# Optimization experiments

Hardware: AMD Instinct MI355X
Metric: run time of the kernel (lower is better)

## Reference

```python
import jax, jax.numpy as jnp
import numpy as np

FEATURE_W = 1.0
TRIPLET_W = 1.0
SOFT_W = 1.0
MARGIN = 0.2
TEMP = 1.0
COMMIT_W = 0.1
DISTORT_W = 0.1
STRIDE = 320

B, T, D, K = 8, 1500, 512, 4096


def setup_inputs() -> dict:
    key = jax.random.key(0)
    k1, k2, k3, k4, k5 = jax.random.split(key, 5)
    return {
        "student_features": jax.random.normal(k1, (B, T, D), dtype=jnp.float32),
        "teacher_features": jax.random.normal(k2, (B, T, D), dtype=jnp.float32),
        "teacher_codes": jax.random.randint(k3, (B, T), 0, K),
        "codebook": jax.random.normal(k4, (K, D), dtype=jnp.float32),
        "lengths": jax.random.randint(k5, (B,), 0, T * STRIDE),
    }


def _sq_dists(flat, codebook):
    x2 = jnp.sum(flat * flat, axis=-1, keepdims=True)          # (N,1)
    c2 = jnp.sum(codebook * codebook, axis=-1)[None, :]        # (1,K)
    xc = jnp.einsum("nd,kd->nk", flat, codebook)               # (N,K)
    return jnp.maximum(x2 + c2 - 2.0 * xc, 0.0)


def reference(student_features, teacher_features, teacher_codes, codebook, lengths):
    b, t, d = student_features.shape
    # valid-frame mask from sample lengths
    valid = jnp.minimum(lengths // STRIDE, t)                  # (B,)
    mask = (jnp.arange(t)[None, :] < valid[:, None]).astype(student_features.dtype)  # (B,T)
    msum = jnp.sum(mask)

    # feature loss: masked mean of per-token MSE
    diff = student_features - teacher_features
    feature_loss = jnp.sum(jnp.mean(diff * diff, axis=-1) * mask) / msum

    # triplet loss
    pos_dist = jnp.sqrt(jnp.sum(diff * diff, axis=-1))
    neg_teacher = jnp.roll(teacher_features, shift=1, axis=0)
    nd = student_features - neg_teacher
    neg_dist = jnp.sqrt(jnp.sum(nd * nd, axis=-1))
    triplet = jax.nn.relu(pos_dist - neg_dist + MARGIN)
    triplet_loss = jnp.sum(triplet * mask) / msum

    # soft token (KL distillation over codebook logits)
    s_flat = student_features.reshape(-1, d)                   # (B*T, D)
    t_flat = teacher_features.reshape(-1, d)
    s_logits = -_sq_dists(s_flat, codebook) / TEMP             # (B*T, K)
    t_logits = -_sq_dists(t_flat, codebook) / TEMP
    s_logp = jax.nn.log_softmax(s_logits, axis=-1)
    t_logp = jax.nn.log_softmax(t_logits, axis=-1)
    t_prob = jax.lax.stop_gradient(jnp.exp(t_logp))
    t_logp = jax.lax.stop_gradient(t_logp)
    kl_per_token = jnp.sum(t_prob * (t_logp - s_logp), axis=-1)  # (B*T,)
    flat_mask = mask.reshape(-1)
    soft_loss = jnp.sum(kl_per_token * flat_mask) / msum

    # VQ commitment / distortion (nearest-code quantization)
    codes = jnp.argmax(s_logits, axis=-1)                       # argmin dist == argmax logits
    quantized = codebook[codes].reshape(b, t, d)
    cdiff = student_features - jax.lax.stop_gradient(quantized)
    commitment_loss = jnp.mean(cdiff * cdiff)
    ddiff = jax.lax.stop_gradient(student_features) - quantized
    distortion_loss = jnp.mean(ddiff * ddiff)

    total = (FEATURE_W * feature_loss + TRIPLET_W * triplet_loss
             + SOFT_W * soft_loss + COMMIT_W * commitment_loss
             + DISTORT_W * distortion_loss)
    return total
```

## Files before the change

### kernel.cpp

```cpp
#include <hip/hip_runtime.h>

typedef unsigned short u16;
typedef unsigned int   u32;
typedef float  f32x16 __attribute__((ext_vector_type(16)));
typedef __bf16 bf16x8 __attribute__((ext_vector_type(8)));

#define B_N   8
#define T_N   1500
#define D_N   512
#define K_N   4096
#define NTOK  12000
#define STRD  320

#define X2S_OFF     0u
#define C2_OFF      49152u
#define FEATP_OFF   65536u
#define TRIPP_OFF   67584u
#define SOFTP2_OFF  69632u
#define COMMP2_OFF  70656u
#define STATEP_OFF  71680u
#define SBF_OFF     557056u
#define TBF_OFF     (557056u + 12288000u)
#define CBBF_OFF    (557056u + 24576000u)


__device__ __forceinline__ u16 f2bf(float x){
  u32 u = __float_as_uint(x);
  u32 r = (u + 0x7fffu + ((u >> 16) & 1u)) >> 16;
  return (u16)r;
}

__device__ __forceinline__ void gl_lds16(const void* g, void* l){
  __builtin_amdgcn_global_load_lds(
      (__attribute__((address_space(1))) void*)(g),
      (__attribute__((address_space(3))) void*)(l),
      16, 0, 0);
}

__device__ __forceinline__ void merge_state(float& m, float& Z, float om, float oZ){
  float nm = fmaxf(m, om);
  Z = Z*__expf(m - nm) + oZ*__expf(om - nm);
  m = nm;
}
__device__ __forceinline__ void merge_stateT(float& m, float& Z, float& A,
                                             float om, float oZ, float oA){
  float nm = fmaxf(m, om);
  float e0 = __expf(m - nm), e1 = __expf(om - nm);
  Z = Z*e0 + oZ*e1; A = A*e0 + oA*e1; m = nm;
}

__global__ __launch_bounds__(256) void prep_feat_kernel(
    const float* __restrict__ s, const float* __restrict__ t,
    const int* __restrict__ lengths,
    u16* __restrict__ sbf, u16* __restrict__ tbf,
    float* __restrict__ x2s, float* __restrict__ featP, float* __restrict__ tripP)
{
  const int tid = threadIdx.x;
  const int w = tid >> 6, lane = tid & 63;
  const int kh = lane >> 5, sp = lane & 31;
  const int tt = blockIdx.x;
  const int n = tt*32 + sp;
  const int b = n / T_N, tok = n - b*T_N;
  const int nr = ((b+7)&7)*T_N + tok;
  const float* srow = s + (size_t)n  * D_N;
  const float* trow = t + (size_t)n  * D_N;
  const float* rrow = t + (size_t)nr * D_N;

  float x2 = 0.f, sd2 = 0.f, nd2 = 0.f;
#pragma unroll
  for (int j = 0; j < 8; ++j){
    const int ks = w*8 + j;
    const int k0 = ks*16 + kh*8;
    float4 s0 = *(const float4*)(srow + k0), s1 = *(const float4*)(srow + k0 + 4);
    float4 t0 = *(const float4*)(trow + k0), t1 = *(const float4*)(trow + k0 + 4);
    float4 r0 = *(const float4*)(rrow + k0), r1 = *(const float4*)(rrow + k0 + 4);
    float sv[8] = {s0.x,s0.y,s0.z,s0.w,s1.x,s1.y,s1.z,s1.w};
    float tv[8] = {t0.x,t0.y,t0.z,t0.w,t1.x,t1.y,t1.z,t1.w};
    float rv[8] = {r0.x,r0.y,r0.z,r0.w,r1.x,r1.y,r1.z,r1.w};
    u16 sb[8], tb[8];
#pragma unroll
    for (int i = 0; i < 8; ++i){
      float d = sv[i] - tv[i]; sd2 += d*d;
      x2 += sv[i]*sv[i];
      float e = sv[i] - rv[i]; nd2 += e*e;
      sb[i] = f2bf(sv[i]); tb[i] = f2bf(tv[i]);
    }
    uint4 spk, tpk;
    spk.x = (u32)sb[0] | ((u32)sb[1] << 16); spk.y = (u32)sb[2] | ((u32)sb[3] << 16);
    spk.z = (u32)sb[4] | ((u32)sb[5] << 16); spk.w = (u32)sb[6] | ((u32)sb[7] << 16);
    tpk.x = (u32)tb[0] | ((u32)tb[1] << 16); tpk.y = (u32)tb[2] | ((u32)tb[3] << 16);
    tpk.z = (u32)tb[4] | ((u32)tb[5] << 16); tpk.w = (u32)tb[6] | ((u32)tb[7] << 16);
    const size_t chunk = ((size_t)tt*32 + ks)*64 + lane;
    ((uint4*)sbf)[chunk] = spk;
    ((uint4*)tbf)[chunk] = tpk;
  }

  x2  += __shfl_xor(x2, 32);
  sd2 += __shfl_xor(sd2, 32);
  nd2 += __shfl_xor(nd2, 32);

  __shared__ float st[3][4][32];
  if (lane < 32){ st[0][w][sp] = x2; st[1][w][sp] = sd2; st[2][w][sp] = nd2; }
  __syncthreads();
  if (tid < 32){
    float X2 = st[0][0][tid]+st[0][1][tid]+st[0][2][tid]+st[0][3][tid];
    float SD = st[1][0][tid]+st[1][1][tid]+st[1][2][tid]+st[1][3][tid];
    float ND = st[2][0][tid]+st[2][1][tid]+st[2][2][tid]+st[2][3][tid];
    int n2 = tt*32 + tid, b2 = n2 / T_N, tk2 = n2 - b2*T_N;
    x2s[n2] = X2;
    int valid = lengths[b2] / STRD; if (valid > T_N) valid = T_N;
    float mf = (tk2 < valid) ? 1.f : 0.f;
    float fp = mf * SD * (1.f/512.f);
    float tp = mf * fmaxf(sqrtf(SD) - sqrtf(ND) + 0.2f, 0.f);
#pragma unroll
    for (int mm = 1; mm < 32; mm <<= 1){ fp += __shfl_xor(fp, mm); tp += __shfl_xor(tp, mm); }
    if (tid == 0){ featP[tt] = fp; tripP[tt] = tp; }
  }
}

__global__ __launch_bounds__(64) void prep_cb_kernel(
    const float* __restrict__ cb, u16* __restrict__ cbbf, float* __restrict__ c2)
{
  const int lane = threadIdx.x, kh = lane >> 5, sp = lane & 31;
  const int ctile = blockIdx.x;
  const int ch = ctile >> 6, ci = (ctile >> 4) & 3, ctg = ctile & 15;
  const int code = ctile*32 + sp;
  const float* crow = cb + (size_t)code * D_N;

  float s2 = 0.f;
#pragma unroll
  for (int stp = 0; stp < 32; ++stp){
    const int kc = stp >> 1, ks2 = stp & 1;
    const int k0 = stp*16 + kh*8;
    float4 c0 = *(const float4*)(crow + k0), c1 = *(const float4*)(crow + k0 + 4);
    float cv[8] = {c0.x,c0.y,c0.z,c0.w,c1.x,c1.y,c1.z,c1.w};
    u16 cbv[8];
#pragma unroll
    for (int i = 0; i < 8; ++i){ s2 += cv[i]*cv[i]; cbv[i] = f2bf(cv[i]); }
    uint4 pk;
    pk.x = (u32)cbv[0] | ((u32)cbv[1] << 16); pk.y = (u32)cbv[2] | ((u32)cbv[3] << 16);
    pk.z = (u32)cbv[4] | ((u32)cbv[5] << 16); pk.w = (u32)cbv[6] | ((u32)cbv[7] << 16);
    const size_t chunk = (size_t)((((ch*4+ci)*16 + kc)*16 + ctg)*2 + ks2)*64 + lane;
    ((uint4*)cbbf)[chunk] = pk;
  }
  s2 += __shfl_xor(s2, 32);
  if (lane < 32) c2[ctile*32 + lane] = s2;
}

__global__ __launch_bounds__(256, 1) void main_kl_kernel(
    const u16* __restrict__ sbf, const u16* __restrict__ tbf,
    const u16* __restrict__ cbbf, const float* __restrict__ c2,
    float* __restrict__ stateP)
{
  __shared__ u16 Bb[2][16384];

  const int tid = threadIdx.x;
  const int w = tid >> 6, lane = tid & 63;
  const int kh = lane >> 5;
  const int tt = blockIdx.x >> 1, ch = blockIdx.x & 1;

  const u16* sA  = sbf  + (size_t)tt*16384;
  const u16* tA  = tbf  + (size_t)tt*16384;
  const u16* cbB = cbbf + (size_t)ch*1048576;

#pragma unroll
  for (int r = 0; r < 8; ++r){
    const int off = (r*256 + tid)*8;
    gl_lds16(cbB + off, &Bb[0][off]);
  }
  bf16x8 fS0 = *(const bf16x8*)(sA + (size_t)0*512 + lane*8);
  bf16x8 fS1 = *(const bf16x8*)(sA + (size_t)1*512 + lane*8);
  bf16x8 fT0 = *(const bf16x8*)(tA + (size_t)0*512 + lane*8);
  bf16x8 fT1 = *(const bf16x8*)(tA + (size_t)1*512 + lane*8);

  float mS = -3e38f, zS = 0.f, mT = -3e38f, zT = 0.f, aa = 0.f;
  f32x16 aS[4], aT[4];

  for (int chunk = 0; chunk < 64; ++chunk){
    const int ci = chunk >> 4, kc = chunk & 15;
    const int p = chunk & 1;
    if (kc == 0){
#pragma unroll
      for (int ct = 0; ct < 4; ++ct)
#pragma unroll
        for (int i = 0; i < 16; ++i){ aS[ct][i] = 0.f; aT[ct][i] = 0.f; }
    }
    __syncthreads();
    if (chunk < 63){
      const u16* src = cbB + (size_t)(chunk+1)*16384;
#pragma unroll
      for (int r = 0; r < 8; ++r){
        const int off = (r*256 + tid)*8;
        gl_lds16(src + off, &Bb[p^1][off]);
      }
    }
    bf16x8 nS0 = fS0, nS1 = fS1, nT0 = fT0, nT1 = fT1;
    if (chunk < 63){
      const size_t ks2 = (size_t)((chunk+1) & 15)*2;
      nS0 = *(const bf16x8*)(sA + ks2*512 + lane*8);
      nS1 = *(const bf16x8*)(sA + (ks2+1)*512 + lane*8);
      nT0 = *(const bf16x8*)(tA + ks2*512 + lane*8);
      nT1 = *(const bf16x8*)(tA + (ks2+1)*512 + lane*8);
    }

    const u16* bp = &Bb[p][0];
#pragma unroll
    for (int ct = 0; ct < 4; ++ct){
      const int ctg = w*4 + ct;
      bf16x8 c0 = *(const bf16x8*)(bp + ctg*1024 + 0*512 + lane*8);
      bf16x8 c1 = *(const bf16x8*)(bp + ctg*1024 + 1*512 + lane*8);
      aS[ct] = __builtin_amdgcn_mfma_f32_32x32x16_bf16(c0, fS0, aS[ct], 0, 0, 0);
      aT[ct] = __builtin_amdgcn_mfma_f32_32x32x16_bf16(c0, fT0, aT[ct], 0, 0, 0);
      aS[ct] = __builtin_amdgcn_mfma_f32_32x32x16_bf16(c1, fS1, aS[ct], 0, 0, 0);
      aT[ct] = __builtin_amdgcn_mfma_f32_32x32x16_bf16(c1, fT1, aT[ct], 0, 0, 0);
    }
    fS0 = nS0; fS1 = nS1; fT0 = nT0; fT1 = nT1;

    if (kc == 15){
#pragma unroll
      for (int ct = 0; ct < 4; ++ct){
        const int ctg = w*4 + ct;
        const float* c2b = c2 + ch*2048 + ci*512 + ctg*32 + kh*4;
        float4 g0 = *(const float4*)(c2b);
        float4 g1 = *(const float4*)(c2b + 8);
        float4 g2 = *(const float4*)(c2b + 16);
        float4 g3 = *(const float4*)(c2b + 24);
        float c2v[16] = {g0.x,g0.y,g0.z,g0.w, g1.x,g1.y,g1.z,g1.w,
                         g2.x,g2.y,g2.z,g2.w, g3.x,g3.y,g3.z,g3.w};
        float sl[16], tl[16];
#pragma unroll
        for (int i = 0; i < 16; ++i){
          sl[i] = 2.0f*aS[ct][i] - c2v[i];
          tl[i] = 2.0f*aT[ct][i] - c2v[i];
        }
        float ms_t = sl[0], mt_t = tl[0];
#pragma unroll
        for (int i = 1; i < 16; ++i){ ms_t = fmaxf(ms_t, sl[i]); mt_t = fmaxf(mt_t, tl[i]); }
        float nmS = fmaxf(mS, ms_t), nmT = fmaxf(mT, mt_t);
        float esS = __expf(mS - nmS), esT = __expf(mT - nmT);
        zS *= esS; zT *= esT; aa *= esT;
#pragma unroll
        for (int i = 0; i < 16; ++i){
          zS += __expf(sl[i] - nmS);
          float e = __expf(tl[i] - nmT);
          zT += e; aa += e*(tl[i] - sl[i]);
        }
        mS = nmS; mT = nmT;
      }
    }
  }

  {
    float om = __shfl_xor(mS, 32), oZ = __shfl_xor(zS, 32);
    merge_state(mS, zS, om, oZ);
    float omt = __shfl_xor(mT, 32), ozt = __shfl_xor(zT, 32), oA = __shfl_xor(aa, 32);
    merge_stateT(mT, zT, aa, omt, ozt, oA);
  }
  __syncthreads();
  float* wst = (float*)&Bb[0][0];
  if (lane < 32){
    float* pw = wst + (w*32 + lane)*5;
    pw[0] = mS; pw[1] = zS; pw[2] = mT; pw[3] = zT; pw[4] = aa;
  }
  __syncthreads();
  if (tid < 32){
    const float* p0 = wst + tid*5;
    float m_s = p0[0], z_s = p0[1], m_t = p0[2], z_t = p0[3], a = p0[4];
#pragma unroll
    for (int ww = 1; ww < 4; ++ww){
      const float* pw = wst + (ww*32 + tid)*5;
      merge_state(m_s, z_s, pw[0], pw[1]);
      merge_stateT(m_t, z_t, a, pw[2], pw[3], pw[4]);
    }
    const int n = tt*32 + tid;
    stateP[0*24000 + ch*12000 + n] = m_s;
    stateP[1*24000 + ch*12000 + n] = z_s;
    stateP[2*24000 + ch*12000 + n] = m_t;
    stateP[3*24000 + ch*12000 + n] = z_t;
    stateP[4*24000 + ch*12000 + n] = a;
  }
}

__global__ __launch_bounds__(256) void merge_kernel(
    const float* __restrict__ stateP, const float* __restrict__ x2s,
    const int* __restrict__ lengths,
    float* __restrict__ softP2, float* __restrict__ commP2)
{
  const int tid = threadIdx.x;
  const int n = blockIdx.x*256 + tid;
  float kl = 0.f, md = 0.f;
  if (n < NTOK){
    float m_s = stateP[0*24000 + n], z_s = stateP[1*24000 + n];
    float m_t = stateP[2*24000 + n], z_t = stateP[3*24000 + n], a = stateP[4*24000 + n];
    merge_state(m_s, z_s, stateP[0*24000 + 12000 + n], stateP[1*24000 + 12000 + n]);
    merge_stateT(m_t, z_t, a, stateP[2*24000 + 12000 + n], stateP[3*24000 + 12000 + n],
                 stateP[4*24000 + 12000 + n]);
    float klv = a / z_t - (m_t + __logf(z_t)) + (m_s + __logf(z_s));
    int b = n / T_N, tk = n - b*T_N;
    int valid = lengths[b] / STRD; if (valid > T_N) valid = T_N;
    kl = (tk < valid) ? klv : 0.f;
    md = fmaxf(x2s[n] - m_s, 0.f);
  }
#pragma unroll
  for (int mm = 1; mm < 64; mm <<= 1){ kl += __shfl_xor(kl, mm); md += __shfl_xor(md, mm); }
  __shared__ float rb[2][4];
  if ((tid & 63) == 0){ rb[0][tid>>6] = kl; rb[1][tid>>6] = md; }
  __syncthreads();
  if (tid == 0){
    softP2[blockIdx.x] = rb[0][0]+rb[0][1]+rb[0][2]+rb[0][3];
    commP2[blockIdx.x] = rb[1][0]+rb[1][1]+rb[1][2]+rb[1][3];
  }
}

__global__ __launch_bounds__(256) void finalize_kernel(
    const float* __restrict__ featP, const float* __restrict__ tripP,
    const float* __restrict__ softP2, const float* __restrict__ commP2,
    const int* __restrict__ lengths, float* __restrict__ out)
{
  const int tid = threadIdx.x;
  double f = 0.0, tr = 0.0, sf = 0.0, cm = 0.0;
  for (int i = tid; i < 375; i += 256){ f += (double)featP[i]; tr += (double)tripP[i]; }
  for (int i = tid; i < 47;  i += 256){ sf += (double)softP2[i]; cm += (double)commP2[i]; }
#pragma unroll
  for (int mm = 1; mm < 64; mm <<= 1){
    f  += __shfl_xor(f,  mm); tr += __shfl_xor(tr, mm);
    sf += __shfl_xor(sf, mm); cm += __shfl_xor(cm, mm);
  }
  __shared__ double red[4][4];
  const int w = tid >> 6, lane = tid & 63;
  if (lane == 0){ red[w][0]=f; red[w][1]=tr; red[w][2]=sf; red[w][3]=cm; }
  __syncthreads();
  if (tid == 0){
    double F=0,TR=0,SF=0,CM=0;
    for (int ww = 0; ww < 4; ++ww){ F+=red[ww][0]; TR+=red[ww][1]; SF+=red[ww][2]; CM+=red[ww][3]; }
    long msum = 0;
    for (int b = 0; b < 8; ++b){ int v = lengths[b] / STRD; if (v > T_N) v = T_N; msum += v; }
    double inv = 1.0 / (double)msum;
    double total = F*inv + TR*inv + SF*inv + 0.2 * CM / ((double)B_N * T_N * D_N);
    out[0] = (float)total;
  }
}

extern "C" void kernel_launch(void* const* d_in, const int* in_sizes, int n_in,
                              void* d_out, int out_size, void* d_ws, size_t ws_size,
                              hipStream_t stream)
{
  const float* s  = (const float*)d_in[0];
  const float* t  = (const float*)d_in[1];
  const float* cb = (const float*)d_in[3];
  const int* lengths = (const int*)d_in[4];

  char* ws = (char*)d_ws;
  float* x2s    = (float*)(ws + X2S_OFF);
  float* c2     = (float*)(ws + C2_OFF);
  float* featP  = (float*)(ws + FEATP_OFF);
  float* tripP  = (float*)(ws + TRIPP_OFF);
  float* softP2 = (float*)(ws + SOFTP2_OFF);
  float* commP2 = (float*)(ws + COMMP2_OFF);
  float* stateP = (float*)(ws + STATEP_OFF);
  u16* sbf  = (u16*)(ws + SBF_OFF);
  u16* tbf  = (u16*)(ws + TBF_OFF);
  u16* cbbf = (u16*)(ws + CBBF_OFF);

  prep_feat_kernel<<<375, 256, 0, stream>>>(s, t, lengths, sbf, tbf, x2s, featP, tripP);
  prep_cb_kernel<<<128, 64, 0, stream>>>(cb, cbbf, c2);
  main_kl_kernel<<<750, 256, 0, stream>>>(sbf, tbf, cbbf, c2, stateP);
  merge_kernel<<<47, 256, 0, stream>>>(stateP, x2s, lengths, softP2, commP2);
  finalize_kernel<<<1, 256, 0, stream>>>(featP, tripP, softP2, commP2, lengths, (float*)d_out);
}
```

Measured before the change: 294.0 us.

## Fuse prep kernels, shrink main-kernel tile for occupancy, merge tail reductions

The two prep kernels become one launch with a block-index split. The feature prep gets a new thread mapping so each lane reads contiguous row segments, and the codebook bf16 layout is re-tiled. The main MFMA kernel halves its per-iteration codebook chunk and accumulator count (two code tiles per wave instead of four) and raises launch bounds to 3 blocks per CU, trading more loop iterations and barriers for higher occupancy and latency hiding. The merge and finalize kernels are fused into a single 1024-thread tail kernel, which removes a launch but runs the 12000-token merge on one block.

```diff
diff --git a/kernel.cpp b/kernel.cpp
--- a/kernel.cpp
+++ b/kernel.cpp
@@ -16,8 +16,6 @@
 #define C2_OFF      49152u
 #define FEATP_OFF   65536u
 #define TRIPP_OFF   67584u
-#define SOFTP2_OFF  69632u
-#define COMMP2_OFF  70656u
 #define STATEP_OFF  71680u
 #define SBF_OFF     557056u
 #define TBF_OFF     (557056u + 12288000u)
@@ -49,110 +47,114 @@
   Z = Z*e0 + oZ*e1; A = A*e0 + oA*e1; m = nm;
 }
 
-__global__ __launch_bounds__(256) void prep_feat_kernel(
+__global__ __launch_bounds__(256) void prep_kernel(
     const float* __restrict__ s, const float* __restrict__ t,
-    const int* __restrict__ lengths,
-    u16* __restrict__ sbf, u16* __restrict__ tbf,
-    float* __restrict__ x2s, float* __restrict__ featP, float* __restrict__ tripP)
+    const float* __restrict__ cb, const int* __restrict__ lengths,
+    u16* __restrict__ sbf, u16* __restrict__ tbf, u16* __restrict__ cbbf,
+    float* __restrict__ x2s, float* __restrict__ c2,
+    float* __restrict__ featP, float* __restrict__ tripP)
 {
   const int tid = threadIdx.x;
   const int w = tid >> 6, lane = tid & 63;
-  const int kh = lane >> 5, sp = lane & 31;
-  const int tt = blockIdx.x;
-  const int n = tt*32 + sp;
-  const int b = n / T_N, tok = n - b*T_N;
-  const int nr = ((b+7)&7)*T_N + tok;
-  const float* srow = s + (size_t)n  * D_N;
-  const float* trow = t + (size_t)n  * D_N;
-  const float* rrow = t + (size_t)nr * D_N;
-
-  float x2 = 0.f, sd2 = 0.f, nd2 = 0.f;
-#pragma unroll
-  for (int j = 0; j < 8; ++j){
-    const int ks = w*8 + j;
-    const int k0 = ks*16 + kh*8;
-    float4 s0 = *(const float4*)(srow + k0), s1 = *(const float4*)(srow + k0 + 4);
-    float4 t0 = *(const float4*)(trow + k0), t1 = *(const float4*)(trow + k0 + 4);
-    float4 r0 = *(const float4*)(rrow + k0), r1 = *(const float4*)(rrow + k0 + 4);
-    float sv[8] = {s0.x,s0.y,s0.z,s0.w,s1.x,s1.y,s1.z,s1.w};
-    float tv[8] = {t0.x,t0.y,t0.z,t0.w,t1.x,t1.y,t1.z,t1.w};
-    float rv[8] = {r0.x,r0.y,r0.z,r0.w,r1.x,r1.y,r1.z,r1.w};
-    u16 sb[8], tb[8];
-#pragma unroll
-    for (int i = 0; i < 8; ++i){
-      float d = sv[i] - tv[i]; sd2 += d*d;
-      x2 += sv[i]*sv[i];
-      float e = sv[i] - rv[i]; nd2 += e*e;
-      sb[i] = f2bf(sv[i]); tb[i] = f2bf(tv[i]);
-    }
-    uint4 spk, tpk;
-    spk.x = (u32)sb[0] | ((u32)sb[1] << 16); spk.y = (u32)sb[2] | ((u32)sb[3] << 16);
-    spk.z = (u32)sb[4] | ((u32)sb[5] << 16); spk.w = (u32)sb[6] | ((u32)sb[7] << 16);
-    tpk.x = (u32)tb[0] | ((u32)tb[1] << 16); tpk.y = (u32)tb[2] | ((u32)tb[3] << 16);
-    tpk.z = (u32)tb[4] | ((u32)tb[5] << 16); tpk.w = (u32)tb[6] | ((u32)tb[7] << 16);
-    const size_t chunk = ((size_t)tt*32 + ks)*64 + lane;
-    ((uint4*)sbf)[chunk] = spk;
-    ((uint4*)tbf)[chunk] = tpk;
-  }
-
-  x2  += __shfl_xor(x2, 32);
-  sd2 += __shfl_xor(sd2, 32);
-  nd2 += __shfl_xor(nd2, 32);
-
-  __shared__ float st[3][4][32];
-  if (lane < 32){ st[0][w][sp] = x2; st[1][w][sp] = sd2; st[2][w][sp] = nd2; }
-  __syncthreads();
-  if (tid < 32){
-    float X2 = st[0][0][tid]+st[0][1][tid]+st[0][2][tid]+st[0][3][tid];
-    float SD = st[1][0][tid]+st[1][1][tid]+st[1][2][tid]+st[1][3][tid];
-    float ND = st[2][0][tid]+st[2][1][tid]+st[2][2][tid]+st[2][3][tid];
-    int n2 = tt*32 + tid, b2 = n2 / T_N, tk2 = n2 - b2*T_N;
-    x2s[n2] = X2;
-    int valid = lengths[b2] / STRD; if (valid > T_N) valid = T_N;
-    float mf = (tk2 < valid) ? 1.f : 0.f;
-    float fp = mf * SD * (1.f/512.f);
-    float tp = mf * fmaxf(sqrtf(SD) - sqrtf(ND) + 0.2f, 0.f);
-#pragma unroll
-    for (int mm = 1; mm < 32; mm <<= 1){ fp += __shfl_xor(fp, mm); tp += __shfl_xor(tp, mm); }
-    if (tid == 0){ featP[tt] = fp; tripP[tt] = tp; }
-  }
-}
-
-__global__ __launch_bounds__(64) void prep_cb_kernel(
-    const float* __restrict__ cb, u16* __restrict__ cbbf, float* __restrict__ c2)
-{
-  const int lane = threadIdx.x, kh = lane >> 5, sp = lane & 31;
-  const int ctile = blockIdx.x;
-  const int ch = ctile >> 6, ci = (ctile >> 4) & 3, ctg = ctile & 15;
-  const int code = ctile*32 + sp;
-  const float* crow = cb + (size_t)code * D_N;
-
-  float s2 = 0.f;
-#pragma unroll
-  for (int stp = 0; stp < 32; ++stp){
-    const int kc = stp >> 1, ks2 = stp & 1;
-    const int k0 = stp*16 + kh*8;
-    float4 c0 = *(const float4*)(crow + k0), c1 = *(const float4*)(crow + k0 + 4);
-    float cv[8] = {c0.x,c0.y,c0.z,c0.w,c1.x,c1.y,c1.z,c1.w};
-    u16 cbv[8];
-#pragma unroll
-    for (int i = 0; i < 8; ++i){ s2 += cv[i]*cv[i]; cbv[i] = f2bf(cv[i]); }
-    uint4 pk;
-    pk.x = (u32)cbv[0] | ((u32)cbv[1] << 16); pk.y = (u32)cbv[2] | ((u32)cbv[3] << 16);
-    pk.z = (u32)cbv[4] | ((u32)cbv[5] << 16); pk.w = (u32)cbv[6] | ((u32)cbv[7] << 16);
-    const size_t chunk = (size_t)((((ch*4+ci)*16 + kc)*16 + ctg)*2 + ks2)*64 + lane;
-    ((uint4*)cbbf)[chunk] = pk;
-  }
-  s2 += __shfl_xor(s2, 32);
-  if (lane < 32) c2[ctile*32 + lane] = s2;
-}
-
-__global__ __launch_bounds__(256, 1) void main_kl_kernel(
+  __shared__ float sred[3][32];
+
+  if (blockIdx.x < 375){
+    const int tt = blockIdx.x;
+    const int t8 = lane >> 3, kpart = lane & 7;
+    const int tokL = w*8 + t8;
+    const int n = tt*32 + tokL;
+    const int b = n / T_N, tok = n - b*T_N;
+    const int nr = ((b+7)&7)*T_N + tok;
+    const float* srow = s + (size_t)n  * D_N;
+    const float* trow = t + (size_t)n  * D_N;
+    const float* rrow = t + (size_t)nr * D_N;
+
+    float x2 = 0.f, sd2 = 0.f, nd2 = 0.f;
+    uint4 sbq[8], tbq[8];
+#pragma unroll
+    for (int q = 0; q < 8; ++q){
+      const int kl = q*64 + kpart*8;
+      float4 a0 = *(const float4*)(srow + kl), a1 = *(const float4*)(srow + kl + 4);
+      float4 b0 = *(const float4*)(trow + kl), b1 = *(const float4*)(trow + kl + 4);
+      float4 r0 = *(const float4*)(rrow + kl), r1 = *(const float4*)(rrow + kl + 4);
+      float sv[8] = {a0.x,a0.y,a0.z,a0.w,a1.x,a1.y,a1.z,a1.w};
+      float tv[8] = {b0.x,b0.y,b0.z,b0.w,b1.x,b1.y,b1.z,b1.w};
+      float rv[8] = {r0.x,r0.y,r0.z,r0.w,r1.x,r1.y,r1.z,r1.w};
+      u16 sb[8], tb[8];
+#pragma unroll
+      for (int i = 0; i < 8; ++i){
+        float d = sv[i] - tv[i]; sd2 += d*d;
+        x2 += sv[i]*sv[i];
+        float e = sv[i] - rv[i]; nd2 += e*e;
+        sb[i] = f2bf(sv[i]); tb[i] = f2bf(tv[i]);
+      }
+      sbq[q].x = (u32)sb[0] | ((u32)sb[1]<<16); sbq[q].y = (u32)sb[2] | ((u32)sb[3]<<16);
+      sbq[q].z = (u32)sb[4] | ((u32)sb[5]<<16); sbq[q].w = (u32)sb[6] | ((u32)sb[7]<<16);
+      tbq[q].x = (u32)tb[0] | ((u32)tb[1]<<16); tbq[q].y = (u32)tb[2] | ((u32)tb[3]<<16);
+      tbq[q].z = (u32)tb[4] | ((u32)tb[5]<<16); tbq[q].w = (u32)tb[6] | ((u32)tb[7]<<16);
+    }
+#pragma unroll
+    for (int q = 0; q < 8; ++q){
+      const int ks = q*4 + (kpart >> 1), kh = kpart & 1;
+      const size_t chunk = ((size_t)tt*32 + ks)*64 + kh*32 + tokL;
+      ((uint4*)sbf)[chunk] = sbq[q];
+      ((uint4*)tbf)[chunk] = tbq[q];
+    }
+#pragma unroll
+    for (int mm = 1; mm < 8; mm <<= 1){
+      x2  += __shfl_xor(x2,  mm);
+      sd2 += __shfl_xor(sd2, mm);
+      nd2 += __shfl_xor(nd2, mm);
+    }
+    if (kpart == 0){ sred[0][tokL] = x2; sred[1][tokL] = sd2; sred[2][tokL] = nd2; }
+    __syncthreads();
+    if (tid < 32){
+      float X2 = sred[0][tid], SD = sred[1][tid], ND = sred[2][tid];
+      int n2 = tt*32 + tid, b2 = n2 / T_N, tk2 = n2 - b2*T_N;
+      x2s[n2] = X2;
+      int valid = lengths[b2] / STRD; if (valid > T_N) valid = T_N;
+      float mf = (tk2 < valid) ? 1.f : 0.f;
+      float fp = mf * SD * (1.f/512.f);
+      float tp = mf * fmaxf(sqrtf(SD) - sqrtf(ND) + 0.2f, 0.f);
+#pragma unroll
+      for (int mm = 1; mm < 32; mm <<= 1){ fp += __shfl_xor(fp, mm); tp += __shfl_xor(tp, mm); }
+      if (tid == 0){ featP[tt] = fp; tripP[tt] = tp; }
+    }
+  } else {
+    const int idx = blockIdx.x - 375;
+    const int ctile = idx*4 + w;
+    const int kh = lane >> 5, sp = lane & 31;
+    const int ch = ctile >> 6, cg = (ctile >> 3) & 7, ctg = ctile & 7;
+    const int code = ctile*32 + sp;
+    const float* crow = cb + (size_t)code * D_N;
+
+    float s2 = 0.f;
+#pragma unroll
+    for (int stp = 0; stp < 32; ++stp){
+      const int kc = stp >> 1, ks2 = stp & 1;
+      const int k0 = stp*16 + kh*8;
+      float4 c0 = *(const float4*)(crow + k0), c1 = *(const float4*)(crow + k0 + 4);
+      float cv[8] = {c0.x,c0.y,c0.z,c0.w,c1.x,c1.y,c1.z,c1.w};
+      u16 cbv[8];
+#pragma unroll
+      for (int i = 0; i < 8; ++i){ s2 += cv[i]*cv[i]; cbv[i] = f2bf(cv[i]); }
+      uint4 pk;
+      pk.x = (u32)cbv[0] | ((u32)cbv[1]<<16); pk.y = (u32)cbv[2] | ((u32)cbv[3]<<16);
+      pk.z = (u32)cbv[4] | ((u32)cbv[5]<<16); pk.w = (u32)cbv[6] | ((u32)cbv[7]<<16);
+      const size_t off = ((size_t)(ch*128 + cg*16 + kc))*8192 + ctg*1024 + ks2*512 + lane*8;
+      *(uint4*)(cbbf + off) = pk;
+    }
+    s2 += __shfl_xor(s2, 32);
+    if (lane < 32) c2[ctile*32 + lane] = s2;
+  }
+}
+
+__global__ __launch_bounds__(256, 3) void main_kl_kernel(
     const u16* __restrict__ sbf, const u16* __restrict__ tbf,
     const u16* __restrict__ cbbf, const float* __restrict__ c2,
     float* __restrict__ stateP)
 {
-  __shared__ u16 Bb[2][16384];
+  __shared__ u16 Bb[2][8192];
 
   const int tid = threadIdx.x;
   const int w = tid >> 6, lane = tid & 63;
@@ -164,63 +166,69 @@
   const u16* cbB = cbbf + (size_t)ch*1048576;
 
 #pragma unroll
-  for (int r = 0; r < 8; ++r){
+  for (int r = 0; r < 4; ++r){
     const int off = (r*256 + tid)*8;
     gl_lds16(cbB + off, &Bb[0][off]);
   }
-  bf16x8 fS0 = *(const bf16x8*)(sA + (size_t)0*512 + lane*8);
-  bf16x8 fS1 = *(const bf16x8*)(sA + (size_t)1*512 + lane*8);
-  bf16x8 fT0 = *(const bf16x8*)(tA + (size_t)0*512 + lane*8);
-  bf16x8 fT1 = *(const bf16x8*)(tA + (size_t)1*512 + lane*8);
+  bf16x8 fS0 = *(const bf16x8*)(sA + lane*8);
+  bf16x8 fS1 = *(const bf16x8*)(sA + 512 + lane*8);
+  bf16x8 fT0 = *(const bf16x8*)(tA + lane*8);
+  bf16x8 fT1 = *(const bf16x8*)(tA + 512 + lane*8);
 
   float mS = -3e38f, zS = 0.f, mT = -3e38f, zT = 0.f, aa = 0.f;
-  f32x16 aS[4], aT[4];
-
-  for (int chunk = 0; chunk < 64; ++chunk){
-    const int ci = chunk >> 4, kc = chunk & 15;
-    const int p = chunk & 1;
+  f32x16 aS0, aS1, aT0, aT1;
+
+  for (int c = 0; c < 128; ++c){
+    const int kc = c & 15, p = c & 1;
     if (kc == 0){
 #pragma unroll
-      for (int ct = 0; ct < 4; ++ct)
-#pragma unroll
-        for (int i = 0; i < 16; ++i){ aS[ct][i] = 0.f; aT[ct][i] = 0.f; }
+      for (int i = 0; i < 16; ++i){ aS0[i]=0.f; aS1[i]=0.f; aT0[i]=0.f; aT1[i]=0.f; }
     }
     __syncthreads();
-    if (chunk < 63){
-      const u16* src = cbB + (size_t)(chunk+1)*16384;
-#pragma unroll
-      for (int r = 0; r < 8; ++r){
+    if (c < 127){
+      const u16* src = cbB + (size_t)(c+1)*8192;
+#pragma unroll
+      for (int r = 0; r < 4; ++r){
         const int off = (r*256 + tid)*8;
         gl_lds16(src + off, &Bb[p^1][off]);
       }
     }
     bf16x8 nS0 = fS0, nS1 = fS1, nT0 = fT0, nT1 = fT1;
-    if (chunk < 63){
-      const size_t ks2 = (size_t)((chunk+1) & 15)*2;
-      nS0 = *(const bf16x8*)(sA + ks2*512 + lane*8);
-      nS1 = *(const bf16x8*)(sA + (ks2+1)*512 + lane*8);
-      nT0 = *(const bf16x8*)(tA + ks2*512 + lane*8);
-      nT1 = *(const bf16x8*)(tA + (ks2+1)*512 + lane*8);
+    if (c < 127){
+      const size_t kb = (size_t)((c+1) & 15) * 1024;
+      nS0 = *(const bf16x8*)(sA + kb + lane*8);
+      nS1 = *(const bf16x8*)(sA + kb + 512 + lane*8);
+      nT0 = *(const bf16x8*)(tA + kb + lane*8);
+      nT1 = *(const bf16x8*)(tA + kb + 512 + lane*8);
     }
 
     const u16* bp = &Bb[p][0];
-#pragma unroll
-    for (int ct = 0; ct < 4; ++ct){
-      const int ctg = w*4 + ct;
-      bf16x8 c0 = *(const bf16x8*)(bp + ctg*1024 + 0*512 + lane*8);
-      bf16x8 c1 = *(const bf16x8*)(bp + ctg*1024 + 1*512 + lane*8);
-      aS[ct] = __builtin_amdgcn_mfma_f32_32x32x16_bf16(c0, fS0, aS[ct], 0, 0, 0);
-      aT[ct] = __builtin_amdgcn_mfma_f32_32x32x16_bf16(c0, fT0, aT[ct], 0, 0, 0);
-      aS[ct] = __builtin_amdgcn_mfma_f32_32x32x16_bf16(c1, fS1, aS[ct], 0, 0, 0);
-      aT[ct] = __builtin_amdgcn_mfma_f32_32x32x16_bf16(c1, fT1, aT[ct], 0, 0, 0);
+    {
+      bf16x8 c0 = *(const bf16x8*)(bp + (w*2+0)*1024 + lane*8);
+      bf16x8 c1 = *(const bf16x8*)(bp + (w*2+0)*1024 + 512 + lane*8);
+      aS0 = __builtin_amdgcn_mfma_f32_32x32x16_bf16(c0, fS0, aS0, 0, 0, 0);
+      aT0 = __builtin_amdgcn_mfma_f32_32x32x16_bf16(c0, fT0, aT0, 0, 0, 0);
+      aS0 = __builtin_amdgcn_mfma_f32_32x32x16_bf16(c1, fS1, aS0, 0, 0, 0);
+      aT0 = __builtin_amdgcn_mfma_f32_32x32x16_bf16(c1, fT1, aT0, 0, 0, 0);
+    }
+    {
+      bf16x8 c0 = *(const bf16x8*)(bp + (w*2+1)*1024 + lane*8);
+      bf16x8 c1 = *(const bf16x8*)(bp + (w*2+1)*1024 + 512 + lane*8);
+      aS1 = __builtin_amdgcn_mfma_f32_32x32x16_bf16(c0, fS0, aS1, 0, 0, 0);
+      aT1 = __builtin_amdgcn_mfma_f32_32x32x16_bf16(c0, fT0, aT1, 0, 0, 0);
+      aS1 = __builtin_amdgcn_mfma_f32_32x32x16_bf16(c1, fS1, aS1, 0, 0, 0);
+      aT1 = __builtin_amdgcn_mfma_f32_32x32x16_bf16(c1, fT1, aT1, 0, 0, 0);
     }
     fS0 = nS0; fS1 = nS1; fT0 = nT0; fT1 = nT1;
 
     if (kc == 15){
-#pragma unroll
-      for (int ct = 0; ct < 4; ++ct){
-        const int ctg = w*4 + ct;
-        const float* c2b = c2 + ch*2048 + ci*512 + ctg*32 + kh*4;
+      const int cg = c >> 4;
+#pragma unroll
+      for (int ct = 0; ct < 2; ++ct){
+        const f32x16& vS = ct ? aS1 : aS0;
+        const f32x16& vT = ct ? aT1 : aT0;
+        const int ctg = w*2 + ct;
+        const float* c2b = c2 + ch*2048 + cg*256 + ctg*32 + kh*4;
         float4 g0 = *(const float4*)(c2b);
         float4 g1 = *(const float4*)(c2b + 8);
         float4 g2 = *(const float4*)(c2b + 16);
@@ -230,8 +238,8 @@
         float sl[16], tl[16];
 #pragma unroll
         for (int i = 0; i < 16; ++i){
-          sl[i] = 2.0f*aS[ct][i] - c2v[i];
-          tl[i] = 2.0f*aT[ct][i] - c2v[i];
+          sl[i] = 2.0f*vS[i] - c2v[i];
+          tl[i] = 2.0f*vT[i] - c2v[i];
         }
         float ms_t = sl[0], mt_t = tl[0];
 #pragma unroll
@@ -281,15 +289,14 @@
   }
 }
 
-__global__ __launch_bounds__(256) void merge_kernel(
+__global__ __launch_bounds__(1024) void tail_kernel(
     const float* __restrict__ stateP, const float* __restrict__ x2s,
-    const int* __restrict__ lengths,
-    float* __restrict__ softP2, float* __restrict__ commP2)
+    const float* __restrict__ featP, const float* __restrict__ tripP,
+    const int* __restrict__ lengths, float* __restrict__ out)
 {
   const int tid = threadIdx.x;
-  const int n = blockIdx.x*256 + tid;
-  float kl = 0.f, md = 0.f;
-  if (n < NTOK){
+  double kl_s = 0.0, md_s = 0.0, f = 0.0, tr = 0.0;
+  for (int n = tid; n < NTOK; n += 1024){
     float m_s = stateP[0*24000 + n], z_s = stateP[1*24000 + n];
     float m_t = stateP[2*24000 + n], z_t = stateP[3*24000 + n], a = stateP[4*24000 + n];
     merge_state(m_s, z_s, stateP[0*24000 + 12000 + n], stateP[1*24000 + 12000 + n]);
@@ -298,45 +305,26 @@
     float klv = a / z_t - (m_t + __logf(z_t)) + (m_s + __logf(z_s));
     int b = n / T_N, tk = n - b*T_N;
     int valid = lengths[b] / STRD; if (valid > T_N) valid = T_N;
-    kl = (tk < valid) ? klv : 0.f;
-    md = fmaxf(x2s[n] - m_s, 0.f);
-  }
-#pragma unroll
-  for (int mm = 1; mm < 64; mm <<= 1){ kl += __shfl_xor(kl, mm); md += __shfl_xor(md, mm); }
-  __shared__ float rb[2][4];
-  if ((tid & 63) == 0){ rb[0][tid>>6] = kl; rb[1][tid>>6] = md; }
+    if (tk < valid) kl_s += (double)klv;
+    md_s += (double)fmaxf(x2s[n] - m_s, 0.f);
+  }
+  for (int i = tid; i < 375; i += 1024){ f += (double)featP[i]; tr += (double)tripP[i]; }
+#pragma unroll
+  for (int mm = 1; mm < 64; mm <<= 1){
+    kl_s += __shfl_xor(kl_s, mm); md_s += __shfl_xor(md_s, mm);
+    f    += __shfl_xor(f,    mm); tr   += __shfl_xor(tr,   mm);
+  }
+  __shared__ double red[16][4];
+  const int w = tid >> 6, lane = tid & 63;
+  if (lane == 0){ red[w][0]=kl_s; red[w][1]=md_s; red[w][2]=f; red[w][3]=tr; }
   __syncthreads();
   if (tid == 0){
-    softP2[blockIdx.x] = rb[0][0]+rb[0][1]+rb[0][2]+rb[0][3];
-    commP2[blockIdx.x] = rb[1][0]+rb[1][1]+rb[1][2]+rb[1][3];
-  }
-}
-
-__global__ __launch_bounds__(256) void finalize_kernel(
-    const float* __restrict__ featP, const float* __restrict__ tripP,
-    const float* __restrict__ softP2, const float* __restrict__ commP2,
-    const int* __restrict__ lengths, float* __restrict__ out)
-{
-  const int tid = threadIdx.x;
-  double f = 0.0, tr = 0.0, sf = 0.0, cm = 0.0;
-  for (int i = tid; i < 375; i += 256){ f += (double)featP[i]; tr += (double)tripP[i]; }
-  for (int i = tid; i < 47;  i += 256){ sf += (double)softP2[i]; cm += (double)commP2[i]; }
-#pragma unroll
-  for (int mm = 1; mm < 64; mm <<= 1){
-    f  += __shfl_xor(f,  mm); tr += __shfl_xor(tr, mm);
-    sf += __shfl_xor(sf, mm); cm += __shfl_xor(cm, mm);
-  }
-  __shared__ double red[4][4];
-  const int w = tid >> 6, lane = tid & 63;
-  if (lane == 0){ red[w][0]=f; red[w][1]=tr; red[w][2]=sf; red[w][3]=cm; }
-  __syncthreads();
-  if (tid == 0){
-    double F=0,TR=0,SF=0,CM=0;
-    for (int ww = 0; ww < 4; ++ww){ F+=red[ww][0]; TR+=red[ww][1]; SF+=red[ww][2]; CM+=red[ww][3]; }
+    double KL=0, MD=0, F=0, TR=0;
+    for (int ww = 0; ww < 16; ++ww){ KL+=red[ww][0]; MD+=red[ww][1]; F+=red[ww][2]; TR+=red[ww][3]; }
     long msum = 0;
     for (int b = 0; b < 8; ++b){ int v = lengths[b] / STRD; if (v > T_N) v = T_N; msum += v; }
     double inv = 1.0 / (double)msum;
-    double total = F*inv + TR*inv + SF*inv + 0.2 * CM / ((double)B_N * T_N * D_N);
+    double total = F*inv + TR*inv + KL*inv + 0.2 * MD / ((double)B_N * T_N * D_N);
     out[0] = (float)total;
   }
 }
@@ -355,16 +343,13 @@
   float* c2     = (float*)(ws + C2_OFF);
   float* featP  = (float*)(ws + FEATP_OFF);
   float* tripP  = (float*)(ws + TRIPP_OFF);
-  float* softP2 = (float*)(ws + SOFTP2_OFF);
-  float* commP2 = (float*)(ws + COMMP2_OFF);
   float* stateP = (float*)(ws + STATEP_OFF);
   u16* sbf  = (u16*)(ws + SBF_OFF);
   u16* tbf  = (u16*)(ws + TBF_OFF);
   u16* cbbf = (u16*)(ws + CBBF_OFF);
 
-  prep_feat_kernel<<<375, 256, 0, stream>>>(s, t, lengths, sbf, tbf, x2s, featP, tripP);
-  prep_cb_kernel<<<128, 64, 0, stream>>>(cb, cbbf, c2);
+  prep_kernel<<<407, 256, 0, stream>>>(s, t, cb, lengths, sbf, tbf, cbbf,
+                                       x2s, c2, featP, tripP);
   main_kl_kernel<<<750, 256, 0, stream>>>(sbf, tbf, cbbf, c2, stateP);
-  merge_kernel<<<47, 256, 0, stream>>>(stateP, x2s, lengths, softP2, commP2);
-  finalize_kernel<<<1, 256, 0, stream>>>(featP, tripP, softP2, commP2, lengths, (float*)d_out);
-}
+  tail_kernel<<<1, 1024, 0, stream>>>(stateP, x2s, featP, tripP, lengths, (float*)d_out);
+}
```

Result: faster. 266.4 us (-9.4%).
